# Optimization experiments

Hardware: AMD Instinct MI355X
Metric: run time of the kernel (lower is better)

Reference implementation:

```python
import jax, jax.numpy as jnp
import numpy as np

T, B, H = 2048, 32, 512

def setup_inputs() -> dict:
    key = jax.random.key(0)
    k1, k2, k3, k4 = jax.random.split(key, 4)
    hidden = jax.random.normal(k1, (1, B, H), dtype=jnp.float32)
    encoder_outputs = jax.random.normal(k2, (T, B, H), dtype=jnp.float32)
    # nn.Linear(2H, H): weight (H, 2H), bias (H,)
    bound = 1.0 / np.sqrt(2 * H)
    W_attn = jax.random.uniform(k3, (H, 2 * H), dtype=jnp.float32, minval=-bound, maxval=bound)
    b_attn = jax.random.uniform(jax.random.fold_in(k3, 1), (H,), dtype=jnp.float32, minval=-bound, maxval=bound)
    stdv = 1.0 / np.sqrt(H)
    v = jax.random.normal(k4, (H,), dtype=jnp.float32) * stdv
    return {"hidden": hidden, "encoder_outputs": encoder_outputs,
            "W_attn": W_attn, "b_attn": b_attn, "v": v}

def reference(hidden, encoder_outputs, W_attn, b_attn, v):
    # hidden: (1,B,H) -> broadcast to (B,T,H); enc: (T,B,H) -> (B,T,H)
    enc = jnp.transpose(encoder_outputs, (1, 0, 2))          # (B,T,H)
    h = jnp.broadcast_to(hidden[0][:, None, :], enc.shape)   # (B,T,H)
    cat = jnp.concatenate([h, enc], axis=2)                  # (B,T,2H)
    energy = jnp.tanh(jnp.einsum('bth,oh->bto', cat, W_attn) + b_attn)  # (B,T,H)
    scores = jnp.einsum('bth,h->bt', energy, v)              # (B,T)
    return jax.nn.softmax(scores, axis=1)[:, None, :]        # (B,1,T)
```

## Files before the change

kernel.cpp:

```cpp
#include <hip/hip_runtime.h>
#include <hip/hip_bf16.h>


#define TT 2048
#define BB 32
#define HH 512

typedef __attribute__((ext_vector_type(8))) short bf16x8;
typedef __attribute__((ext_vector_type(4))) float f32x4;

static __device__ __forceinline__ unsigned cvt2(float a, float b) {
    union { __hip_bfloat162 h; unsigned u; } cv;
    cv.h = __float22bfloat162_rn(make_float2(a, b));
    return cv.u;
}

static __device__ __forceinline__ unsigned short f2bf(float f) {
    unsigned int u = __float_as_uint(f);
    unsigned int r = (u + 0x7FFFu + ((u >> 16) & 1u)) >> 16;
    return (unsigned short)r;
}

static __device__ __forceinline__ float fast_tanh(float x) {
    float e = __expf(2.0f * x);
    return 1.0f - 2.0f * __builtin_amdgcn_rcpf(1.0f + e);
}

static __device__ __forceinline__ void gload_lds16(const void* g, void* l) {
    __builtin_amdgcn_global_load_lds(
        (const __attribute__((address_space(1))) unsigned int*)g,
        (__attribute__((address_space(3))) unsigned int*)l, 16, 0, 0);
}

__global__ void pack_w2_kernel(const float* __restrict__ W, short* __restrict__ W2p) {
    int idx = blockIdx.x * 256 + threadIdx.x;
    int nt = idx >> 16;
    int ks = (idx >> 13) & 7;
    int s  = idx & 8191;
    int j  = s >> 6;
    int c  = s & 63;
    int kk = c ^ ((j & 7) << 3);
    int o  = nt * 128 + j;
    int k  = ks * 64 + kk;
    W2p[idx] = (short)f2bf(W[o * 1024 + 512 + k]);
}

__global__ void hb_kernel(const float* __restrict__ hidden, const float* __restrict__ W,
                          const float* __restrict__ b_attn, float* __restrict__ hb) {
    __shared__ float hrow[512];
    int b = blockIdx.x >> 1;
    int o = ((blockIdx.x & 1) << 8) + threadIdx.x;
    for (int h = threadIdx.x; h < 512; h += 256) hrow[h] = hidden[b * 512 + h];
    __syncthreads();
    const float4* wr = reinterpret_cast<const float4*>(W + (size_t)o * 1024);
    const float4* hr = reinterpret_cast<const float4*>(hrow);
    float acc = b_attn[o];
#pragma unroll 8
    for (int i = 0; i < 128; ++i) {
        float4 w = wr[i], h4 = hr[i];
        acc += w.x * h4.x + w.y * h4.y + w.z * h4.z + w.w * h4.w;
    }
    hb[b * 512 + o] = acc;
}

__global__ __launch_bounds__(256, 2) void attn_main_kernel(
    const float* __restrict__ enc, const short* __restrict__ W2p,
    const float* __restrict__ hb, const float* __restrict__ v,
    float* __restrict__ scores_part)
{
    __shared__ short As[2][128 * 64];
    __shared__ short Bs[2][128 * 64];
    __shared__ float s_red[2][128];

    const int tid = threadIdx.x;
    const int bid = blockIdx.x;
    const int w = (bid & 7) * 256 + (bid >> 3);
    const int nt = w & 3;
    const int mtile = w >> 2;
    const int b = mtile >> 4;
    const int t0 = (mtile & 15) * 128;

    const int wave = tid >> 6;
    const int lane = tid & 63;
    const int wr = wave >> 1;
    const int wc = wave & 1;
    const int lcol = lane & 15;
    const int lq = lane >> 4;

    const int arow = tid >> 3;
    const int afc = (tid & 7) * 8;
    const short* bsrc = W2p + nt * 65536 + (wave * 4) * 512 + lane * 8;

    f32x4 acc[4][4];
#pragma unroll
    for (int mt = 0; mt < 4; ++mt)
#pragma unroll
        for (int ns = 0; ns < 4; ++ns) acc[mt][ns] = (f32x4){0.f, 0.f, 0.f, 0.f};

    float4 rA[8];

#define A_LOAD(KS)                                                                  \
    {                                                                               \
        _Pragma("unroll")                                                           \
        for (int p = 0; p < 4; ++p) {                                               \
            const int r = p * 32 + arow;                                            \
            const float* src = enc + ((size_t)(t0 + r) * BB + b) * HH + (KS) * 64 + afc; \
            rA[p * 2]     = *reinterpret_cast<const float4*>(src);                  \
            rA[p * 2 + 1] = *reinterpret_cast<const float4*>(src + 4);              \
        }                                                                           \
    }

#define B_STAGE(KS, BUF)                                                            \
    {                                                                               \
        const short* s0 = bsrc + (KS) * 8192;                                       \
        _Pragma("unroll")                                                           \
        for (int c = 0; c < 4; ++c)                                                 \
            gload_lds16(s0 + c * 512, &Bs[BUF][(wave * 4 + c) * 512]);              \
    }

#define A_WRITE(BUF)                                                                \
    {                                                                               \
        _Pragma("unroll")                                                           \
        for (int p = 0; p < 4; ++p) {                                               \
            const int r = p * 32 + arow;                                            \
            uint4 pk;                                                               \
            pk.x = cvt2(rA[p * 2].x, rA[p * 2].y);                                  \
            pk.y = cvt2(rA[p * 2].z, rA[p * 2].w);                                  \
            pk.z = cvt2(rA[p * 2 + 1].x, rA[p * 2 + 1].y);                          \
            pk.w = cvt2(rA[p * 2 + 1].z, rA[p * 2 + 1].w);                          \
            const int cs = afc ^ ((r & 7) << 3);                                    \
            *reinterpret_cast<uint4*>(&As[BUF][r * 64 + cs]) = pk;                  \
        }                                                                           \
    }

#define COMPUTE(BUF)                                                                \
    {                                                                               \
        _Pragma("unroll")                                                           \
        for (int ksub = 0; ksub < 2; ++ksub) {                                      \
            const int kk = ksub * 32 + lq * 8;                                      \
            bf16x8 af[4], bfr[4];                                                   \
            _Pragma("unroll")                                                       \
            for (int mt = 0; mt < 4; ++mt) {                                        \
                const int r = wr * 64 + mt * 16 + lcol;                             \
                af[mt] = *reinterpret_cast<const bf16x8*>(                          \
                    &As[BUF][r * 64 + (kk ^ ((r & 7) << 3))]);                      \
            }                                                                       \
            _Pragma("unroll")                                                       \
            for (int ns = 0; ns < 4; ++ns) {                                        \
                const int j = wc * 64 + ns * 16 + lcol;                             \
                bfr[ns] = *reinterpret_cast<const bf16x8*>(                         \
                    &Bs[BUF][j * 64 + (kk ^ ((j & 7) << 3))]);                      \
            }                                                                       \
            _Pragma("unroll")                                                       \
            for (int mt = 0; mt < 4; ++mt)                                          \
                _Pragma("unroll")                                                   \
                for (int ns = 0; ns < 4; ++ns)                                      \
                    acc[mt][ns] = __builtin_amdgcn_mfma_f32_16x16x32_bf16(          \
                        af[mt], bfr[ns], acc[mt][ns], 0, 0, 0);                     \
        }                                                                           \
    }

    A_LOAD(0);
    B_STAGE(0, 0);
    A_WRITE(0);
    __syncthreads();

    for (int ks = 0; ks < 8; ++ks) {
        const int cur = ks & 1;
        if (ks < 7) {
            A_LOAD(ks + 1);
            B_STAGE(ks + 1, cur ^ 1);
        }
        COMPUTE(cur);
        if (ks < 7) {
            A_WRITE(cur ^ 1);
            __syncthreads();
        }
    }

    float part[4][4];
#pragma unroll
    for (int mt = 0; mt < 4; ++mt)
#pragma unroll
        for (int j = 0; j < 4; ++j) part[mt][j] = 0.0f;

#pragma unroll
    for (int ns = 0; ns < 4; ++ns) {
        const int o = nt * 128 + wc * 64 + ns * 16 + lcol;
        const float hbv = hb[b * 512 + o];
        const float vv = v[o];
#pragma unroll
        for (int mt = 0; mt < 4; ++mt)
#pragma unroll
            for (int j = 0; j < 4; ++j)
                part[mt][j] = fmaf(fast_tanh(acc[mt][ns][j] + hbv), vv, part[mt][j]);
    }

#pragma unroll
    for (int off = 1; off < 16; off <<= 1)
#pragma unroll
        for (int mt = 0; mt < 4; ++mt)
#pragma unroll
            for (int j = 0; j < 4; ++j)
                part[mt][j] += __shfl_xor(part[mt][j], off, 64);

    if (lcol == 0) {
#pragma unroll
        for (int mt = 0; mt < 4; ++mt)
#pragma unroll
            for (int j = 0; j < 4; ++j)
                s_red[wc][wr * 64 + mt * 16 + lq * 4 + j] = part[mt][j];
    }
    __syncthreads();

    if (tid < 128)
        scores_part[((size_t)nt * BB + b) * TT + t0 + tid] =
            s_red[0][tid] + s_red[1][tid];
}

__global__ void softmax_kernel(const float* __restrict__ sp, float* __restrict__ out) {
    __shared__ float wred[4];
    __shared__ float wsum[4];
    const int b = blockIdx.x;
    const int tid = threadIdx.x;
    float vals[8];
    float mx = -1e30f;
#pragma unroll
    for (int i = 0; i < 8; ++i) {
        const int t = i * 256 + tid;
        const float s = sp[(size_t)b * TT + t] + sp[((size_t)BB + b) * TT + t] +
                        sp[((size_t)2 * BB + b) * TT + t] + sp[((size_t)3 * BB + b) * TT + t];
        vals[i] = s;
        mx = fmaxf(mx, s);
    }
#pragma unroll
    for (int off = 32; off; off >>= 1) mx = fmaxf(mx, __shfl_xor(mx, off, 64));
    if ((tid & 63) == 0) wred[tid >> 6] = mx;
    __syncthreads();
    mx = fmaxf(fmaxf(wred[0], wred[1]), fmaxf(wred[2], wred[3]));
    float s = 0.0f;
#pragma unroll
    for (int i = 0; i < 8; ++i) {
        vals[i] = __expf(vals[i] - mx);
        s += vals[i];
    }
#pragma unroll
    for (int off = 32; off; off >>= 1) s += __shfl_xor(s, off, 64);
    if ((tid & 63) == 0) wsum[tid >> 6] = s;
    __syncthreads();
    s = wsum[0] + wsum[1] + wsum[2] + wsum[3];
    const float inv = 1.0f / s;
#pragma unroll
    for (int i = 0; i < 8; ++i) out[b * TT + i * 256 + tid] = vals[i] * inv;
}

extern "C" void kernel_launch(void* const* d_in, const int* in_sizes, int n_in,
                              void* d_out, int out_size, void* d_ws, size_t ws_size,
                              hipStream_t stream) {
    const float* hidden = (const float*)d_in[0];
    const float* enc    = (const float*)d_in[1];
    const float* W      = (const float*)d_in[2];
    const float* b_attn = (const float*)d_in[3];
    const float* v      = (const float*)d_in[4];
    float* out = (float*)d_out;

    char* base = (char*)d_ws;
    short* W2p = (short*)base;
    float* hb  = (float*)(base + 524288);
    float* sp  = (float*)(base + 524288 + 65536);

    pack_w2_kernel<<<1024, 256, 0, stream>>>(W, W2p);
    hb_kernel<<<64, 256, 0, stream>>>(hidden, W, b_attn, hb);
    attn_main_kernel<<<2048, 256, 0, stream>>>(enc, W2p, hb, v, sp);
    softmax_kernel<<<32, 256, 0, stream>>>(sp, out);
}
```

Before: 89.85 us.

## Deepen A-tile register prefetch to two stages and fully unroll K loop

Adds a second register buffer for the fp32 encoder tile so global loads for step k+2 are issued while step k computes, giving each load about two compute phases to land. The K loop is unrolled by two with fixed LDS buffer indices, and the base address is hoisted out of the loads. The cost is extra VGPRs (another 8 float4 per thread), which on top of the 64 accumulator registers may lower occupancy or cause spills.

```diff
diff --git a/kernel.cpp b/kernel.cpp
--- a/kernel.cpp
+++ b/kernel.cpp
@@ -89,6 +89,7 @@
 
     const int arow = tid >> 3;
     const int afc = (tid & 7) * 8;
+    const float* encbase = enc + ((size_t)(t0 + arow) * BB + b) * HH + afc;
     const short* bsrc = W2p + nt * 65536 + (wave * 4) * 512 + lane * 8;
 
     f32x4 acc[4][4];
@@ -97,16 +98,15 @@
 #pragma unroll
         for (int ns = 0; ns < 4; ++ns) acc[mt][ns] = (f32x4){0.f, 0.f, 0.f, 0.f};
 
-    float4 rA[8];
-
-#define A_LOAD(KS)                                                                  \
+    float4 rA0[8], rA1[8];
+
+#define A_LOAD(RA, KS)                                                              \
     {                                                                               \
         _Pragma("unroll")                                                           \
         for (int p = 0; p < 4; ++p) {                                               \
-            const int r = p * 32 + arow;                                            \
-            const float* src = enc + ((size_t)(t0 + r) * BB + b) * HH + (KS) * 64 + afc; \
-            rA[p * 2]     = *reinterpret_cast<const float4*>(src);                  \
-            rA[p * 2 + 1] = *reinterpret_cast<const float4*>(src + 4);              \
+            const float* src = encbase + (size_t)p * 32 * BB * HH + (KS) * 64;      \
+            RA[p * 2]     = *reinterpret_cast<const float4*>(src);                  \
+            RA[p * 2 + 1] = *reinterpret_cast<const float4*>(src + 4);              \
         }                                                                           \
     }
 
@@ -118,16 +118,16 @@
             gload_lds16(s0 + c * 512, &Bs[BUF][(wave * 4 + c) * 512]);              \
     }
 
-#define A_WRITE(BUF)                                                                \
+#define A_WRITE(RA, BUF)                                                            \
     {                                                                               \
         _Pragma("unroll")                                                           \
         for (int p = 0; p < 4; ++p) {                                               \
             const int r = p * 32 + arow;                                            \
             uint4 pk;                                                               \
-            pk.x = cvt2(rA[p * 2].x, rA[p * 2].y);                                  \
-            pk.y = cvt2(rA[p * 2].z, rA[p * 2].w);                                  \
-            pk.z = cvt2(rA[p * 2 + 1].x, rA[p * 2 + 1].y);                          \
-            pk.w = cvt2(rA[p * 2 + 1].z, rA[p * 2 + 1].w);                          \
+            pk.x = cvt2(RA[p * 2].x, RA[p * 2].y);                                  \
+            pk.y = cvt2(RA[p * 2].z, RA[p * 2].w);                                  \
+            pk.z = cvt2(RA[p * 2 + 1].x, RA[p * 2 + 1].y);                          \
+            pk.w = cvt2(RA[p * 2 + 1].z, RA[p * 2 + 1].w);                          \
             const int cs = afc ^ ((r & 7) << 3);                                    \
             *reinterpret_cast<uint4*>(&As[BUF][r * 64 + cs]) = pk;                  \
         }                                                                           \
@@ -160,20 +160,25 @@
         }                                                                           \
     }
 
-    A_LOAD(0);
+    A_LOAD(rA0, 0);
     B_STAGE(0, 0);
-    A_WRITE(0);
-    __syncthreads();
-
-    for (int ks = 0; ks < 8; ++ks) {
-        const int cur = ks & 1;
-        if (ks < 7) {
-            A_LOAD(ks + 1);
-            B_STAGE(ks + 1, cur ^ 1);
-        }
-        COMPUTE(cur);
-        if (ks < 7) {
-            A_WRITE(cur ^ 1);
+    A_WRITE(rA0, 0);
+    A_LOAD(rA1, 1);
+    __syncthreads();
+
+#pragma unroll
+    for (int s2 = 0; s2 < 4; ++s2) {
+        const int s = s2 * 2;
+        if (s + 2 < 8) A_LOAD(rA0, s + 2);
+        B_STAGE(s + 1, 1);
+        COMPUTE(0);
+        A_WRITE(rA1, 1);
+        __syncthreads();
+        if (s + 3 < 8) A_LOAD(rA1, s + 3);
+        if (s + 2 < 8) B_STAGE(s + 2, 0);
+        COMPUTE(1);
+        if (s + 2 < 8) {
+            A_WRITE(rA0, 0);
             __syncthreads();
         }
     }
```

Result: faster. 83.49 us (-7.1%).
